# Kernel optimization log

Hardware: AMD Instinct MI355X
Metric: run time of the kernel (lower is better)

## Reference

```python
import jax, jax.numpy as jnp
import numpy as np
from jax import lax

EPS = 1e-5
NBIT = 127.0  # 8-bit symmetric: 2^(8-1)-1

def ste_round(x):
    return x + lax.stop_gradient(jnp.round(x) - x)

def quant_act(x, rng_max):
    # symmetric fake-quant of activations with learned per-cluster range
    s = rng_max / NBIT
    xq = jnp.clip(ste_round(x / s), -NBIT, NBIT) * s
    return xq, s

def fold_bn(w, gamma, beta, mean, var):
    std = jnp.sqrt(var + EPS)
    scale = gamma / std
    w_f = w * scale[:, None, None, None]
    b_f = beta - mean * scale
    return w_f, b_f

def quant_weight(w):
    # per-output-channel symmetric quant
    s = jnp.max(jnp.abs(w), axis=(1, 2, 3), keepdims=True) / NBIT
    wq = jnp.clip(ste_round(w / s), -NBIT, NBIT) * s
    return wq, s.reshape(-1)

def conv(x, w, stride=1, groups=1, pad=0):
    return lax.conv_general_dilated(
        x, w, window_strides=(stride, stride),
        padding=((pad, pad), (pad, pad)),
        dimension_numbers=('NCHW', 'OIHW', 'NCHW'),
        feature_group_count=groups)

def setup_inputs() -> dict:
    key = jax.random.key(0)
    ks = jax.random.split(key, 24)
    B, Cin, H, W = 64, 96, 28, 28
    Cmid, Cout, NC = 576, 96, 4
    d = {}
    d['x'] = jax.random.normal(ks[0], (B, Cin, H, W), dtype=jnp.float32)
    # conv1: 1x1 expansion
    d['w1'] = jax.random.normal(ks[1], (Cmid, Cin, 1, 1), jnp.float32) * 0.1
    d['g1'] = jax.random.uniform(ks[2], (Cmid,), minval=0.5, maxval=1.5)
    d['b1'] = jax.random.normal(ks[3], (Cmid,)) * 0.1
    d['m1'] = jax.random.normal(ks[4], (Cmid,)) * 0.1
    d['v1'] = jax.random.uniform(ks[5], (Cmid,), minval=0.5, maxval=1.5)
    # conv2: 3x3 depthwise
    d['w2'] = jax.random.normal(ks[6], (Cmid, 1, 3, 3), jnp.float32) * 0.1
    d['g2'] = jax.random.uniform(ks[7], (Cmid,), minval=0.5, maxval=1.5)
    d['b2'] = jax.random.normal(ks[8], (Cmid,)) * 0.1
    d['m2'] = jax.random.normal(ks[9], (Cmid,)) * 0.1
    d['v2'] = jax.random.uniform(ks[10], (Cmid,), minval=0.5, maxval=1.5)
    # conv3: 1x1 projection
    d['w3'] = jax.random.normal(ks[11], (Cout, Cmid, 1, 1), jnp.float32) * 0.1
    d['g3'] = jax.random.uniform(ks[12], (Cout,), minval=0.5, maxval=1.5)
    d['b3'] = jax.random.normal(ks[13], (Cout,)) * 0.1
    d['m3'] = jax.random.normal(ks[14], (Cout,)) * 0.1
    d['v3'] = jax.random.uniform(ks[15], (Cout,), minval=0.5, maxval=1.5)
    # per-cluster learned activation ranges for the 4 QuantAct modules
    d['r0'] = jax.random.uniform(ks[16], (NC,), minval=2.0, maxval=8.0)
    d['r1'] = jax.random.uniform(ks[17], (NC,), minval=2.0, maxval=8.0)
    d['r2'] = jax.random.uniform(ks[18], (NC,), minval=2.0, maxval=8.0)
    d['r3'] = jax.random.uniform(ks[19], (NC,), minval=2.0, maxval=8.0)
    d['cluster'] = 2
    return d

def reference(x, w1, g1, b1, m1, v1, w2, g2, b2, m2, v2,
              w3, g3, b3, m3, v3, r0, r1, r2, r3, cluster):
    identity = x  # residual path (in==out, stride==1)
    # QuantAct -> conv1 (BN-folded, per-channel quant) -> ReLU6
    xq, s0 = quant_act(x, r0[cluster])
    w1f, bf1 = fold_bn(w1, g1, b1, m1, v1)
    w1q, ws1 = quant_weight(w1f)
    y = conv(xq, w1q) + bf1[None, :, None, None]
    y = jnp.clip(y, 0.0, 6.0)
    # QuantAct1 -> depthwise conv2 -> ReLU6
    yq, s1 = quant_act(y, r1[cluster])
    w2f, bf2 = fold_bn(w2, g2, b2, m2, v2)
    w2q, ws2 = quant_weight(w2f)
    y = conv(yq, w2q, stride=1, groups=w2.shape[0], pad=1) + bf2[None, :, None, None]
    y = jnp.clip(y, 0.0, 6.0)
    # QuantAct2 -> conv3 projection
    yq, s2 = quant_act(y, r2[cluster])
    w3f, bf3 = fold_bn(w3, g3, b3, m3, v3)
    w3q, ws3 = quant_weight(w3f)
    y = conv(yq, w3q) + bf3[None, :, None, None]
    # residual add, then int32 requant
    y = y + identity
    out, s3 = quant_act(y, r3[cluster])
    return out, s3
```

## Files before the change

kernel.cpp:

```cpp
#include <hip/hip_runtime.h>
#include <cstdint>
#include <cstddef>

typedef int   v4i __attribute__((ext_vector_type(4)));
typedef float v4f __attribute__((ext_vector_type(4)));
typedef unsigned int u32;

constexpr int B_   = 64;
constexpr int CIN  = 96;
constexpr int P_   = 784;
constexpr int CMID = 576;
constexpr int COUT = 96;
constexpr int NOUT = B_ * COUT * P_;
constexpr float NBITF = 127.0f;
constexpr float EPSF  = 1e-5f;
constexpr float MAGICF = 12582912.0f;
constexpr int   BIASI  = 0x4B400000;

constexpr int XKD = 36;
constexpr int XBD = 13 * XKD * 64;

__device__ __forceinline__ int dot3(u32 a, u32 w, int acc) {
#if __has_builtin(__builtin_amdgcn_sdot4)
    return __builtin_amdgcn_sdot4((int)a, (int)w, acc, false);
#else
    return acc + (int)(signed char)(a)        * (int)(signed char)(w)
               + (int)(signed char)(a >> 8)   * (int)(signed char)(w >> 8)
               + (int)(signed char)(a >> 16)  * (int)(signed char)(w >> 16);
#endif
}

__device__ __forceinline__ void tr4(u32 S0, u32 S1, u32 S2, u32 S3, u32 O[4]) {
    u32 u01 = __builtin_amdgcn_perm(S1, S0, 0x05010400u);
    u32 u23 = __builtin_amdgcn_perm(S3, S2, 0x05010400u);
    u32 v01 = __builtin_amdgcn_perm(S1, S0, 0x07030602u);
    u32 v23 = __builtin_amdgcn_perm(S3, S2, 0x07030602u);
    O[0] = __builtin_amdgcn_perm(u23, u01, 0x05040100u);
    O[1] = __builtin_amdgcn_perm(u23, u01, 0x07060302u);
    O[2] = __builtin_amdgcn_perm(v23, v01, 0x05040100u);
    O[3] = __builtin_amdgcn_perm(v23, v01, 0x07060302u);
}

__device__ __forceinline__ u32 pack4(u32 t0, u32 t1, u32 t2, u32 t3) {
    u32 p01 = __builtin_amdgcn_perm(t1, t0, 0x05010400u);
    u32 p23 = __builtin_amdgcn_perm(t3, t2, 0x05010400u);
    return __builtin_amdgcn_perm(p23, p01, 0x05040100u);
}

__global__ __launch_bounds__(64)
void prep_weights(const float* __restrict__ w1, const float* __restrict__ g1,
                  const float* __restrict__ b1, const float* __restrict__ m1,
                  const float* __restrict__ v1,
                  const float* __restrict__ w2, const float* __restrict__ g2,
                  const float* __restrict__ b2, const float* __restrict__ m2,
                  const float* __restrict__ v2,
                  const float* __restrict__ w3, const float* __restrict__ g3,
                  const float* __restrict__ b3, const float* __restrict__ m3,
                  const float* __restrict__ v3,
                  int8_t* __restrict__ w1qp, float* __restrict__ ws1, float* __restrict__ bf1,
                  v4i* __restrict__ w2pk, float* __restrict__ ws2, float* __restrict__ bf2,
                  int8_t* __restrict__ w3qp, float* __restrict__ ws3, float* __restrict__ bf3)
{
    int blk  = blockIdx.x;
    int lane = threadIdx.x;

    const float *w, *g, *bb, *mm, *vv;
    int oc, K, which;
    if (blk < CMID)            { which = 0; w = w1; g = g1; bb = b1; mm = m1; vv = v1; oc = blk;            K = CIN;  }
    else if (blk < 2 * CMID)   { which = 1; w = w2; g = g2; bb = b2; mm = m2; vv = v2; oc = blk - CMID;     K = 9;    }
    else                       { which = 2; w = w3; g = g3; bb = b3; mm = m3; vv = v3; oc = blk - 2 * CMID; K = CMID; }

    float scale = g[oc] / sqrtf(vv[oc] + EPSF);

    float mx = 0.f;
    for (int k = lane; k < K; k += 64)
        mx = fmaxf(mx, fabsf(w[oc * K + k] * scale));
    #pragma unroll
    for (int off = 1; off < 64; off <<= 1)
        mx = fmaxf(mx, __shfl_xor(mx, off));

    float s = mx / NBITF;

    int myq = 0;
    for (int k = lane; k < K; k += 64) {
        float wf = w[oc * K + k] * scale;
        float q  = fminf(fmaxf(rintf(wf / s), -127.f), 127.f);
        if (which == 0)      w1qp[oc * 144 + k] = (int8_t)q;
        else if (which == 1) myq = (int)q;
        else                 w3qp[oc * 592 + k] = (int8_t)q;
    }
    if (which == 0 && lane < 12)
        ((u32*)(w1qp + oc * 144))[24 + lane] = 0u;
    if (which == 1) {
        u32 qq[9];
        #pragma unroll
        for (int t = 0; t < 9; t++) qq[t] = (u32)__shfl(myq, t, 64) & 0xffu;
        if (lane == 0) {
            v4i pk;
            pk[0] = (int)(qq[0] | (qq[1] << 8) | (qq[2] << 16));
            pk[1] = (int)(qq[3] | (qq[4] << 8) | (qq[5] << 16));
            pk[2] = (int)(qq[6] | (qq[7] << 8) | (qq[8] << 16));
            pk[3] = 0;
            w2pk[oc] = pk;
        }
    }
    if (lane == 0) {
        float bf = bb[oc] - mm[oc] * scale;
        if (which == 0)      { ws1[oc] = s; bf1[oc] = bf; }
        else if (which == 1) { ws2[oc] = s; bf2[oc] = bf; }
        else                 { ws3[oc] = s; bf3[oc] = bf; }
    }
}

__global__ __launch_bounds__(256)
void quant_x(const float* __restrict__ x, const float* __restrict__ r0,
             const int* __restrict__ cluster, u32* __restrict__ x8t)
{
    __shared__ u32 T[112 * 37];

    int tid = threadIdx.x, pt0 = blockIdx.x, b = blockIdx.y;
    float inv_s0 = NBITF / r0[cluster[0]];

    for (int i = tid; i < 112 * 12; i += 256) {
        int row = i / 12, cpad = i - row * 12;
        T[row * 37 + 24 + cpad] = 0u;
    }
    for (int u = tid; u < 24 * 28; u += 256) {
        int pq = u % 28, icq = u / 28;
        int pxb = pt0 * 112 + pq * 4;
        int q[4][4];
        #pragma unroll
        for (int j = 0; j < 4; j++) {
            v4f xv = *(const v4f*)(x + ((size_t)b * CIN + icq * 4 + j) * P_ + pxb);
            #pragma unroll
            for (int i = 0; i < 4; i++)
                q[j][i] = (int)fminf(fmaxf(rintf(xv[i] * inv_s0), -127.f), 127.f);
        }
        #pragma unroll
        for (int i = 0; i < 4; i++) {
            u32 t0 = __builtin_amdgcn_perm((u32)q[1][i], (u32)q[0][i], 0x00000400u);
            u32 t1 = __builtin_amdgcn_perm((u32)q[3][i], (u32)q[2][i], 0x00000400u);
            T[(pq * 4 + i) * 37 + icq] = __builtin_amdgcn_perm(t1, t0, 0x05040100u);
        }
    }
    __syncthreads();
    u32* gb = x8t + (size_t)b * XBD;
    for (int i = tid; i < XKD * 112; i += 256) {
        int icq = i / 112, pxo = i - icq * 112;
        int px = pt0 * 112 + pxo;
        gb[(((px >> 6) * XKD) + icq) * 64 + (px & 63)] = T[pxo * 37 + icq];
    }
}

__global__ __launch_bounds__(256)
void conv1s(const u32* __restrict__ x8t, const int8_t* __restrict__ w1qp,
            const float* __restrict__ ws1, const float* __restrict__ bf1,
            const float* __restrict__ r0, const float* __restrict__ r1,
            const int* __restrict__ cluster, u32* __restrict__ y1px)
{
    int tid = threadIdx.x, b = blockIdx.y;
    int mt = blockIdx.x % 3, pt = blockIdx.x / 3;
    int p0 = pt * 64;
    int lane = tid & 63, wv = tid >> 6;
    int n = lane & 15, q4 = lane >> 4;
    int ocw = mt * 192 + wv * 48;

    int   c      = cluster[0];
    float s0     = r0[c] / NBITF;
    float inv_s1 = NBITF / r1[c];
    int   u1i    = (int)fminf(rintf(6.f * inv_s1), 127.f);

    const u32* xb = x8t + (size_t)b * XBD;
    int abase[4];
    #pragma unroll
    for (int jm = 0; jm < 4; jm++) {
        int px = p0 + 16 * jm + n;
        px = min(px, P_ - 1);
        abase[jm] = ((px >> 6) * XKD) * 64 + (px & 63);
    }

    v4i acc[3][4];
    #pragma unroll
    for (int jn = 0; jn < 3; jn++)
        #pragma unroll
        for (int jm = 0; jm < 4; jm++) acc[jn][jm] = (v4i){0, 0, 0, 0};

    const v4i* w4 = (const v4i*)w1qp;
    #pragma unroll
    for (int ks = 0; ks < 2; ks++) {
        v4i bfr[3], afr[4];
        #pragma unroll
        for (int jn = 0; jn < 3; jn++) {
            int oc = ocw + 16 * jn + n;
            bfr[jn] = w4[oc * 9 + ks * 4 + q4];
        }
        #pragma unroll
        for (int jm = 0; jm < 4; jm++) {
            int kb = (16 * ks + 4 * q4) * 64;
            u32 d0 = xb[abase[jm] + kb];
            u32 d1 = xb[abase[jm] + kb + 64];
            u32 d2 = xb[abase[jm] + kb + 128];
            u32 d3 = xb[abase[jm] + kb + 192];
            afr[jm] = (v4i){(int)d0, (int)d1, (int)d2, (int)d3};
        }
        #pragma unroll
        for (int jn = 0; jn < 3; jn++)
            #pragma unroll
            for (int jm = 0; jm < 4; jm++)
                acc[jn][jm] = __builtin_amdgcn_mfma_i32_16x16x64_i8(afr[jm], bfr[jn], acc[jn][jm], 0, 0, 0);
    }

    #pragma unroll
    for (int jn = 0; jn < 3; jn++) {
        int   oc  = ocw + 16 * jn + n;
        float scv = s0 * ws1[oc] * inv_s1;
        float bbv = bf1[oc] * inv_s1;
        size_t rowbase = (size_t)(b * CMID + oc) * 196 + (p0 >> 2);
        #pragma unroll
        for (int jm = 0; jm < 4; jm++) {
            int quad = p0 + 16 * jm + 4 * q4;
            u32 t[4];
            #pragma unroll
            for (int r = 0; r < 4; r++) {
                float f = fmaf((float)acc[jn][jm][r], scv, bbv) + MAGICF;
                int v = __float_as_int(f);
                t[r] = (u32)min(max(v, BIASI), BIASI + u1i);
            }
            if (quad < P_)
                y1px[rowbase + 4 * jm + q4] = pack4(t[0], t[1], t[2], t[3]);
        }
    }
}

__global__ __launch_bounds__(256)
void conv2s(const u32* __restrict__ y1px, const v4i* __restrict__ w2pk,
            const float* __restrict__ ws2, const float* __restrict__ bf2,
            const float* __restrict__ r1, const float* __restrict__ r2,
            const int* __restrict__ cluster, u32* __restrict__ y2px)
{
    int gid = blockIdx.x * 256 + threadIdx.x;
    int r  = gid % 28;
    int t  = gid / 28;
    int ch = t % CMID;
    int b  = t / CMID;

    int   c      = cluster[0];
    float s1     = r1[c] / NBITF;
    float inv_s2 = NBITF / r2[c];
    int   u2i    = (int)fminf(rintf(6.f * inv_s2), 127.f);

    const u32* base = y1px + (size_t)(b * CMID + ch) * 196;
    u32 R[3][7];
    #pragma unroll
    for (int dr = 0; dr < 3; dr++) {
        int rr = r + dr - 1;
        bool ok = (unsigned)rr < 28u;
        #pragma unroll
        for (int j = 0; j < 7; j++)
            R[dr][j] = ok ? base[rr * 7 + j] : 0u;
    }

    v4i wpk = w2pk[ch];
    u32 pk0 = (u32)wpk[0], pk1 = (u32)wpk[1], pk2 = (u32)wpk[2];
    float scv = s1 * ws2[ch] * inv_s2;
    float bbv = bf2[ch] * inv_s2;

    u32* orow = y2px + (size_t)(b * CMID + ch) * 196 + r * 7;
    #pragma unroll
    for (int j = 0; j < 7; j++) {
        int a0 = 0, a1 = 0, a2 = 0, a3 = 0;
        #pragma unroll
        for (int dr = 0; dr < 3; dr++) {
            u32 D   = R[dr][j];
            u32 Dm1 = (j > 0) ? R[dr][j - 1] : 0u;
            u32 Dp1 = (j < 6) ? R[dr][j + 1] : 0u;
            u32 pk  = (dr == 0) ? pk0 : (dr == 1) ? pk1 : pk2;
            a0 = dot3(__builtin_amdgcn_alignbyte(D, Dm1, 3), pk, a0);
            a1 = dot3(D, pk, a1);
            a2 = dot3(__builtin_amdgcn_alignbyte(Dp1, D, 1), pk, a2);
            a3 = dot3(__builtin_amdgcn_alignbyte(Dp1, D, 2), pk, a3);
        }
        int aa[4] = {a0, a1, a2, a3};
        u32 tq[4];
        #pragma unroll
        for (int i = 0; i < 4; i++) {
            float f = fmaf((float)aa[i], scv, bbv) + MAGICF;
            int v = __float_as_int(f);
            tq[i] = (u32)min(max(v, BIASI), BIASI + u2i);
        }
        orow[j] = pack4(tq[0], tq[1], tq[2], tq[3]);
    }
}

__global__ __launch_bounds__(256)
void conv3s(const u32* __restrict__ y2px, const int8_t* __restrict__ w3qp,
            const float* __restrict__ ws3, const float* __restrict__ bf3,
            const float* __restrict__ x, const float* __restrict__ r2,
            const float* __restrict__ r3, const int* __restrict__ cluster,
            float* __restrict__ out)
{
    __shared__ u32 Bsh[144 * 67];

    int tid = threadIdx.x, b = blockIdx.y, pt = blockIdx.x;
    int p0d = pt * 16;

    int   c      = cluster[0];
    float s2     = r2[c] / NBITF;
    float s3     = r3[c] / NBITF;
    float inv_s3 = NBITF / r3[c];

    for (int u = tid; u < 2304; u += 256) {
        int pxq = u & 15, chq = u >> 4;
        u32 S[4];
        #pragma unroll
        for (int r = 0; r < 4; r++) {
            int col = min(p0d + pxq, 195);
            S[r] = y2px[(size_t)(b * CMID + 4 * chq + r) * 196 + col];
        }
        u32 O[4];
        tr4(S[0], S[1], S[2], S[3], O);
        #pragma unroll
        for (int k = 0; k < 4; k++)
            Bsh[chq * 67 + 4 * pxq + k] = O[k];
    }
    __syncthreads();

    int lane = tid & 63, wv = tid >> 6;
    int n = lane & 15, q4 = lane >> 4;
    int pxl = wv * 16 + n;

    v4i acc[6];
    #pragma unroll
    for (int i = 0; i < 6; i++) acc[i] = (v4i){0, 0, 0, 0};

    #pragma unroll
    for (int ks = 0; ks < 9; ks++) {
        int kr = 16 * ks + 4 * q4;
        u32 b0 = Bsh[(kr + 0) * 67 + pxl];
        u32 b1 = Bsh[(kr + 1) * 67 + pxl];
        u32 b2 = Bsh[(kr + 2) * 67 + pxl];
        u32 b3 = Bsh[(kr + 3) * 67 + pxl];
        v4i bfr = (v4i){(int)b0, (int)b1, (int)b2, (int)b3};
        #pragma unroll
        for (int i = 0; i < 6; i++) {
            v4i afr = *(const v4i*)(w3qp + (size_t)(i * 16 + n) * 592 + ks * 64 + q4 * 16);
            acc[i] = __builtin_amdgcn_mfma_i32_16x16x64_i8(afr, bfr, acc[i], 0, 0, 0);
        }
    }

    int px = pt * 64 + pxl;
    if (px < P_) {
        #pragma unroll
        for (int i = 0; i < 6; i++) {
            #pragma unroll
            for (int r = 0; r < 4; r++) {
                int oc = i * 16 + q4 * 4 + r;
                size_t gi = (size_t)(b * COUT + oc) * P_ + px;
                float v  = (float)acc[i][r] * (s2 * ws3[oc]) + bf3[oc] + x[gi];
                float f  = fmaf(v, inv_s3, MAGICF);
                int lvl  = min(max(__float_as_int(f) - BIASI, -127), 127);
                out[gi]  = (float)lvl * s3;
            }
        }
    }
    if (pt == 0 && b == 0 && tid == 0)
        out[NOUT] = s3;
}

extern "C" void kernel_launch(void* const* d_in, const int* in_sizes, int n_in,
                              void* d_out, int out_size, void* d_ws, size_t ws_size,
                              hipStream_t stream)
{
    const float* x  = (const float*)d_in[0];
    const float* w1 = (const float*)d_in[1];
    const float* g1 = (const float*)d_in[2];
    const float* b1 = (const float*)d_in[3];
    const float* m1 = (const float*)d_in[4];
    const float* v1 = (const float*)d_in[5];
    const float* w2 = (const float*)d_in[6];
    const float* g2 = (const float*)d_in[7];
    const float* b2 = (const float*)d_in[8];
    const float* m2 = (const float*)d_in[9];
    const float* v2 = (const float*)d_in[10];
    const float* w3 = (const float*)d_in[11];
    const float* g3 = (const float*)d_in[12];
    const float* b3 = (const float*)d_in[13];
    const float* m3 = (const float*)d_in[14];
    const float* v3 = (const float*)d_in[15];
    const float* r0 = (const float*)d_in[16];
    const float* r1 = (const float*)d_in[17];
    const float* r2 = (const float*)d_in[18];
    const float* r3 = (const float*)d_in[19];
    const int*   cl = (const int*)d_in[20];

    float* out = (float*)d_out;

    char*  ws  = (char*)d_ws;
    size_t off = 0;
    auto carve = [&](size_t bytes) {
        size_t cur = off;
        off = (off + bytes + 255) & ~(size_t)255;
        return (void*)(ws + cur);
    };
    int8_t* w1qp = (int8_t*)carve((size_t)CMID * 144);
    float*  ws1  = (float*)carve(CMID * 4);
    float*  bf1  = (float*)carve(CMID * 4);
    v4i*    w2pk = (v4i*)carve((size_t)CMID * 16);
    float*  ws2  = (float*)carve(CMID * 4);
    float*  bf2  = (float*)carve(CMID * 4);
    int8_t* w3qp = (int8_t*)carve((size_t)COUT * 592);
    float*  ws3  = (float*)carve(COUT * 4);
    float*  bf3  = (float*)carve(COUT * 4);
    u32*    y1px = (u32*)carve((size_t)B_ * CMID * 196 * 4);
    u32*    y2px = (u32*)carve((size_t)B_ * CMID * 196 * 4);
    u32*    x8t  = y2px;
    (void)ws_size; (void)in_sizes; (void)n_in; (void)out_size;

    prep_weights<<<dim3(2 * CMID + COUT), dim3(64), 0, stream>>>(
        w1, g1, b1, m1, v1, w2, g2, b2, m2, v2, w3, g3, b3, m3, v3,
        w1qp, ws1, bf1, w2pk, ws2, bf2, w3qp, ws3, bf3);

    quant_x<<<dim3(7, B_), dim3(256), 0, stream>>>(x, r0, cl, x8t);

    conv1s<<<dim3(39, B_), dim3(256), 0, stream>>>(
        x8t, w1qp, ws1, bf1, r0, r1, cl, y1px);

    conv2s<<<dim3((B_ * CMID * 28) / 256), dim3(256), 0, stream>>>(
        y1px, w2pk, ws2, bf2, r1, r2, cl, y2px);

    conv3s<<<dim3(13, B_), dim3(256), 0, stream>>>(
        y2px, w3qp, ws3, bf3, x, r2, r3, cl, out);
}
```

Baseline: 187.7 us.

## Fuse conv1 and depthwise conv2 via shared-memory halo, merge prep kernels

Merges the weight-prep and input-quantization kernels into one launch, and fuses the 1x1 expansion conv with the 3x3 depthwise conv. Each block computes conv1 on a 64-pixel tile widened by a 32-pixel halo on each side, stores the int8 results in shared memory, and runs the depthwise stencil directly from there. This removes the global round trip of the 576-channel intermediate and two launches. In exchange, conv1 work roughly doubles per block from the recomputed halo, and register and shared-memory pressure rise.

```diff
diff --git a/kernel.cpp b/kernel.cpp
--- a/kernel.cpp
+++ b/kernel.cpp
@@ -47,22 +47,64 @@
     return __builtin_amdgcn_perm(p23, p01, 0x05040100u);
 }
 
-__global__ __launch_bounds__(64)
-void prep_weights(const float* __restrict__ w1, const float* __restrict__ g1,
-                  const float* __restrict__ b1, const float* __restrict__ m1,
-                  const float* __restrict__ v1,
-                  const float* __restrict__ w2, const float* __restrict__ g2,
-                  const float* __restrict__ b2, const float* __restrict__ m2,
-                  const float* __restrict__ v2,
-                  const float* __restrict__ w3, const float* __restrict__ g3,
-                  const float* __restrict__ b3, const float* __restrict__ m3,
-                  const float* __restrict__ v3,
-                  int8_t* __restrict__ w1qp, float* __restrict__ ws1, float* __restrict__ bf1,
-                  v4i* __restrict__ w2pk, float* __restrict__ ws2, float* __restrict__ bf2,
-                  int8_t* __restrict__ w3qp, float* __restrict__ ws3, float* __restrict__ bf3)
+__global__ __launch_bounds__(256)
+void prep_all(const float* __restrict__ x,
+              const float* __restrict__ w1, const float* __restrict__ g1,
+              const float* __restrict__ b1, const float* __restrict__ m1,
+              const float* __restrict__ v1,
+              const float* __restrict__ w2, const float* __restrict__ g2,
+              const float* __restrict__ b2, const float* __restrict__ m2,
+              const float* __restrict__ v2,
+              const float* __restrict__ w3, const float* __restrict__ g3,
+              const float* __restrict__ b3, const float* __restrict__ m3,
+              const float* __restrict__ v3,
+              const float* __restrict__ r0, const int* __restrict__ cluster,
+              u32* __restrict__ x8t,
+              int8_t* __restrict__ w1qp, float* __restrict__ ws1, float* __restrict__ bf1,
+              v4i* __restrict__ w2pk, float* __restrict__ ws2, float* __restrict__ bf2,
+              int8_t* __restrict__ w3qp, float* __restrict__ ws3, float* __restrict__ bf3)
 {
-    int blk  = blockIdx.x;
-    int lane = threadIdx.x;
+    __shared__ u32 T[112 * 37];
+    int tid = threadIdx.x;
+
+    if (blockIdx.x < 448) {
+        int pt0 = blockIdx.x % 7, b = blockIdx.x / 7;
+        float inv_s0 = NBITF / r0[cluster[0]];
+
+        for (int i = tid; i < 112 * 12; i += 256) {
+            int row = i / 12, cpad = i - row * 12;
+            T[row * 37 + 24 + cpad] = 0u;
+        }
+        for (int u = tid; u < 24 * 28; u += 256) {
+            int pq = u % 28, icq = u / 28;
+            int pxb = pt0 * 112 + pq * 4;
+            int q[4][4];
+            #pragma unroll
+            for (int j = 0; j < 4; j++) {
+                v4f xv = *(const v4f*)(x + ((size_t)b * CIN + icq * 4 + j) * P_ + pxb);
+                #pragma unroll
+                for (int i = 0; i < 4; i++)
+                    q[j][i] = (int)fminf(fmaxf(rintf(xv[i] * inv_s0), -127.f), 127.f);
+            }
+            #pragma unroll
+            for (int i = 0; i < 4; i++) {
+                u32 t0 = __builtin_amdgcn_perm((u32)q[1][i], (u32)q[0][i], 0x00000400u);
+                u32 t1 = __builtin_amdgcn_perm((u32)q[3][i], (u32)q[2][i], 0x00000400u);
+                T[(pq * 4 + i) * 37 + icq] = __builtin_amdgcn_perm(t1, t0, 0x05040100u);
+            }
+        }
+        __syncthreads();
+        u32* gb = x8t + (size_t)b * XBD;
+        for (int i = tid; i < XKD * 112; i += 256) {
+            int icq = i / 112, pxo = i - icq * 112;
+            int px = pt0 * 112 + pxo;
+            gb[(((px >> 6) * XKD) + icq) * 64 + (px & 63)] = T[pxo * 37 + icq];
+        }
+        return;
+    }
+
+    int lane = tid & 63, wv = tid >> 6;
+    int blk = (blockIdx.x - 448) * 4 + wv;
 
     const float *w, *g, *bb, *mm, *vv;
     int oc, K, which;
@@ -113,51 +155,16 @@
 }
 
 __global__ __launch_bounds__(256)
-void quant_x(const float* __restrict__ x, const float* __restrict__ r0,
-             const int* __restrict__ cluster, u32* __restrict__ x8t)
+void conv12v2(const u32* __restrict__ x8t, const int8_t* __restrict__ w1qp,
+              const float* __restrict__ ws1, const float* __restrict__ bf1,
+              const v4i* __restrict__ w2pk, const float* __restrict__ ws2,
+              const float* __restrict__ bf2,
+              const float* __restrict__ r0, const float* __restrict__ r1,
+              const float* __restrict__ r2, const int* __restrict__ cluster,
+              u32* __restrict__ y2px)
 {
-    __shared__ u32 T[112 * 37];
-
-    int tid = threadIdx.x, pt0 = blockIdx.x, b = blockIdx.y;
-    float inv_s0 = NBITF / r0[cluster[0]];
-
-    for (int i = tid; i < 112 * 12; i += 256) {
-        int row = i / 12, cpad = i - row * 12;
-        T[row * 37 + 24 + cpad] = 0u;
-    }
-    for (int u = tid; u < 24 * 28; u += 256) {
-        int pq = u % 28, icq = u / 28;
-        int pxb = pt0 * 112 + pq * 4;
-        int q[4][4];
-        #pragma unroll
-        for (int j = 0; j < 4; j++) {
-            v4f xv = *(const v4f*)(x + ((size_t)b * CIN + icq * 4 + j) * P_ + pxb);
-            #pragma unroll
-            for (int i = 0; i < 4; i++)
-                q[j][i] = (int)fminf(fmaxf(rintf(xv[i] * inv_s0), -127.f), 127.f);
-        }
-        #pragma unroll
-        for (int i = 0; i < 4; i++) {
-            u32 t0 = __builtin_amdgcn_perm((u32)q[1][i], (u32)q[0][i], 0x00000400u);
-            u32 t1 = __builtin_amdgcn_perm((u32)q[3][i], (u32)q[2][i], 0x00000400u);
-            T[(pq * 4 + i) * 37 + icq] = __builtin_amdgcn_perm(t1, t0, 0x05040100u);
-        }
-    }
-    __syncthreads();
-    u32* gb = x8t + (size_t)b * XBD;
-    for (int i = tid; i < XKD * 112; i += 256) {
-        int icq = i / 112, pxo = i - icq * 112;
-        int px = pt0 * 112 + pxo;
-        gb[(((px >> 6) * XKD) + icq) * 64 + (px & 63)] = T[pxo * 37 + icq];
-    }
-}
-
-__global__ __launch_bounds__(256)
-void conv1s(const u32* __restrict__ x8t, const int8_t* __restrict__ w1qp,
-            const float* __restrict__ ws1, const float* __restrict__ bf1,
-            const float* __restrict__ r0, const float* __restrict__ r1,
-            const int* __restrict__ cluster, u32* __restrict__ y1px)
-{
+    __shared__ u32 y1w[192 * 34];
+
     int tid = threadIdx.x, b = blockIdx.y;
     int mt = blockIdx.x % 3, pt = blockIdx.x / 3;
     int p0 = pt * 64;
@@ -167,128 +174,111 @@
 
     int   c      = cluster[0];
     float s0     = r0[c] / NBITF;
+    float s1     = r1[c] / NBITF;
     float inv_s1 = NBITF / r1[c];
+    float inv_s2 = NBITF / r2[c];
     int   u1i    = (int)fminf(rintf(6.f * inv_s1), 127.f);
+    int   u2i    = (int)fminf(rintf(6.f * inv_s2), 127.f);
 
     const u32* xb = x8t + (size_t)b * XBD;
-    int abase[4];
-    #pragma unroll
-    for (int jm = 0; jm < 4; jm++) {
-        int px = p0 + 16 * jm + n;
-        px = min(px, P_ - 1);
+    int abase[8];
+    #pragma unroll
+    for (int jm = 0; jm < 8; jm++) {
+        int px = p0 - 32 + 16 * jm + n;
+        px = min(max(px, 0), P_ - 1);
         abase[jm] = ((px >> 6) * XKD) * 64 + (px & 63);
     }
 
-    v4i acc[3][4];
+    v4i acc[3][8];
     #pragma unroll
     for (int jn = 0; jn < 3; jn++)
         #pragma unroll
-        for (int jm = 0; jm < 4; jm++) acc[jn][jm] = (v4i){0, 0, 0, 0};
+        for (int jm = 0; jm < 8; jm++) acc[jn][jm] = (v4i){0, 0, 0, 0};
 
     const v4i* w4 = (const v4i*)w1qp;
     #pragma unroll
     for (int ks = 0; ks < 2; ks++) {
-        v4i bfr[3], afr[4];
+        v4i bfr[3];
         #pragma unroll
         for (int jn = 0; jn < 3; jn++) {
             int oc = ocw + 16 * jn + n;
             bfr[jn] = w4[oc * 9 + ks * 4 + q4];
         }
-        #pragma unroll
-        for (int jm = 0; jm < 4; jm++) {
-            int kb = (16 * ks + 4 * q4) * 64;
+        int kb = (16 * ks + 4 * q4) * 64;
+        #pragma unroll
+        for (int jm = 0; jm < 8; jm++) {
             u32 d0 = xb[abase[jm] + kb];
             u32 d1 = xb[abase[jm] + kb + 64];
             u32 d2 = xb[abase[jm] + kb + 128];
             u32 d3 = xb[abase[jm] + kb + 192];
-            afr[jm] = (v4i){(int)d0, (int)d1, (int)d2, (int)d3};
-        }
-        #pragma unroll
-        for (int jn = 0; jn < 3; jn++)
+            v4i afr = (v4i){(int)d0, (int)d1, (int)d2, (int)d3};
             #pragma unroll
-            for (int jm = 0; jm < 4; jm++)
-                acc[jn][jm] = __builtin_amdgcn_mfma_i32_16x16x64_i8(afr[jm], bfr[jn], acc[jn][jm], 0, 0, 0);
+            for (int jn = 0; jn < 3; jn++)
+                acc[jn][jm] = __builtin_amdgcn_mfma_i32_16x16x64_i8(afr, bfr[jn], acc[jn][jm], 0, 0, 0);
+        }
     }
 
     #pragma unroll
     for (int jn = 0; jn < 3; jn++) {
         int   oc  = ocw + 16 * jn + n;
+        int   chl = wv * 48 + 16 * jn + n;
         float scv = s0 * ws1[oc] * inv_s1;
         float bbv = bf1[oc] * inv_s1;
-        size_t rowbase = (size_t)(b * CMID + oc) * 196 + (p0 >> 2);
-        #pragma unroll
-        for (int jm = 0; jm < 4; jm++) {
-            int quad = p0 + 16 * jm + 4 * q4;
+        #pragma unroll
+        for (int jm = 0; jm < 8; jm++) {
             u32 t[4];
             #pragma unroll
             for (int r = 0; r < 4; r++) {
+                int wpx = p0 - 32 + 16 * jm + 4 * q4 + r;
                 float f = fmaf((float)acc[jn][jm][r], scv, bbv) + MAGICF;
-                int v = __float_as_int(f);
-                t[r] = (u32)min(max(v, BIASI), BIASI + u1i);
+                int v = min(max(__float_as_int(f), BIASI), BIASI + u1i);
+                t[r] = ((unsigned)wpx < (unsigned)P_) ? (u32)v : (u32)BIASI;
             }
-            if (quad < P_)
-                y1px[rowbase + 4 * jm + q4] = pack4(t[0], t[1], t[2], t[3]);
-        }
-    }
-}
-
-__global__ __launch_bounds__(256)
-void conv2s(const u32* __restrict__ y1px, const v4i* __restrict__ w2pk,
-            const float* __restrict__ ws2, const float* __restrict__ bf2,
-            const float* __restrict__ r1, const float* __restrict__ r2,
-            const int* __restrict__ cluster, u32* __restrict__ y2px)
-{
-    int gid = blockIdx.x * 256 + threadIdx.x;
-    int r  = gid % 28;
-    int t  = gid / 28;
-    int ch = t % CMID;
-    int b  = t / CMID;
-
-    int   c      = cluster[0];
-    float s1     = r1[c] / NBITF;
-    float inv_s2 = NBITF / r2[c];
-    int   u2i    = (int)fminf(rintf(6.f * inv_s2), 127.f);
-
-    const u32* base = y1px + (size_t)(b * CMID + ch) * 196;
-    u32 R[3][7];
-    #pragma unroll
-    for (int dr = 0; dr < 3; dr++) {
-        int rr = r + dr - 1;
-        bool ok = (unsigned)rr < 28u;
-        #pragma unroll
-        for (int j = 0; j < 7; j++)
-            R[dr][j] = ok ? base[rr * 7 + j] : 0u;
-    }
-
-    v4i wpk = w2pk[ch];
-    u32 pk0 = (u32)wpk[0], pk1 = (u32)wpk[1], pk2 = (u32)wpk[2];
-    float scv = s1 * ws2[ch] * inv_s2;
-    float bbv = bf2[ch] * inv_s2;
-
-    u32* orow = y2px + (size_t)(b * CMID + ch) * 196 + r * 7;
-    #pragma unroll
-    for (int j = 0; j < 7; j++) {
+            y1w[chl * 34 + 4 * jm + q4] = pack4(t[0], t[1], t[2], t[3]);
+        }
+    }
+    __syncthreads();
+
+    int d0g = p0 >> 2;
+    #pragma unroll
+    for (int it = 0; it < 12; it++) {
+        int u   = tid + 256 * it;
+        int chl = u >> 4, dq = u & 15;
+        int d   = d0g + dq;
+        int gcol = d % 7;
+        int base = chl * 34 + 8 + dq;
+
+        u32 M[3][3];
+        #pragma unroll
+        for (int rr = 0; rr < 3; rr++) {
+            int o = (rr - 1) * 7;
+            M[rr][0] = (gcol == 0) ? 0u : y1w[base + o - 1];
+            M[rr][1] = y1w[base + o];
+            M[rr][2] = (gcol == 6) ? 0u : y1w[base + o + 1];
+        }
+        int ch = mt * 192 + chl;
+        v4i wpk = w2pk[ch];
         int a0 = 0, a1 = 0, a2 = 0, a3 = 0;
         #pragma unroll
-        for (int dr = 0; dr < 3; dr++) {
-            u32 D   = R[dr][j];
-            u32 Dm1 = (j > 0) ? R[dr][j - 1] : 0u;
-            u32 Dp1 = (j < 6) ? R[dr][j + 1] : 0u;
-            u32 pk  = (dr == 0) ? pk0 : (dr == 1) ? pk1 : pk2;
+        for (int rr = 0; rr < 3; rr++) {
+            u32 Dm1 = M[rr][0], D = M[rr][1], Dp1 = M[rr][2];
+            u32 pk = (u32)((rr == 0) ? wpk[0] : (rr == 1) ? wpk[1] : wpk[2]);
             a0 = dot3(__builtin_amdgcn_alignbyte(D, Dm1, 3), pk, a0);
             a1 = dot3(D, pk, a1);
             a2 = dot3(__builtin_amdgcn_alignbyte(Dp1, D, 1), pk, a2);
             a3 = dot3(__builtin_amdgcn_alignbyte(Dp1, D, 2), pk, a3);
         }
+        float scv = s1 * ws2[ch] * inv_s2;
+        float bbv = bf2[ch] * inv_s2;
         int aa[4] = {a0, a1, a2, a3};
         u32 tq[4];
         #pragma unroll
         for (int i = 0; i < 4; i++) {
             float f = fmaf((float)aa[i], scv, bbv) + MAGICF;
-            int v = __float_as_int(f);
-            tq[i] = (u32)min(max(v, BIASI), BIASI + u2i);
-        }
-        orow[j] = pack4(tq[0], tq[1], tq[2], tq[3]);
+            tq[i] = (u32)min(max(__float_as_int(f), BIASI), BIASI + u2i);
+        }
+        if (d < 196)
+            y2px[(size_t)(b * CMID + ch) * 196 + d] = pack4(tq[0], tq[1], tq[2], tq[3]);
     }
 }
 
@@ -411,22 +401,17 @@
     int8_t* w3qp = (int8_t*)carve((size_t)COUT * 592);
     float*  ws3  = (float*)carve(COUT * 4);
     float*  bf3  = (float*)carve(COUT * 4);
-    u32*    y1px = (u32*)carve((size_t)B_ * CMID * 196 * 4);
+    u32*    x8t  = (u32*)carve((size_t)B_ * XBD * 4);
     u32*    y2px = (u32*)carve((size_t)B_ * CMID * 196 * 4);
-    u32*    x8t  = y2px;
     (void)ws_size; (void)in_sizes; (void)n_in; (void)out_size;
 
-    prep_weights<<<dim3(2 * CMID + COUT), dim3(64), 0, stream>>>(
-        w1, g1, b1, m1, v1, w2, g2, b2, m2, v2, w3, g3, b3, m3, v3,
+    prep_all<<<dim3(760), dim3(256), 0, stream>>>(
+        x, w1, g1, b1, m1, v1, w2, g2, b2, m2, v2, w3, g3, b3, m3, v3,
+        r0, cl, x8t,
         w1qp, ws1, bf1, w2pk, ws2, bf2, w3qp, ws3, bf3);
 
-    quant_x<<<dim3(7, B_), dim3(256), 0, stream>>>(x, r0, cl, x8t);
-
-    conv1s<<<dim3(39, B_), dim3(256), 0, stream>>>(
-        x8t, w1qp, ws1, bf1, r0, r1, cl, y1px);
-
-    conv2s<<<dim3((B_ * CMID * 28) / 256), dim3(256), 0, stream>>>(
-        y1px, w2pk, ws2, bf2, r1, r2, cl, y2px);
+    conv12v2<<<dim3(39, B_), dim3(256), 0, stream>>>(
+        x8t, w1qp, ws1, bf1, w2pk, ws2, bf2, r0, r1, r2, cl, y2px);
 
     conv3s<<<dim3(13, B_), dim3(256), 0, stream>>>(
         y2px, w3qp, ws3, bf3, x, r2, r3, cl, out);
```

Result: no change. 188.8 us (+0.6%).
